# Performance work log

Measured on AMD Instinct MI355X. Metric: run time of the kernel, lower is better.

The kernel has to match this reference:

```python
import jax, jax.numpy as jnp
import numpy as np

DIM = 768
NUM_BLOCKS = 4
BLOCK = DIM // NUM_BLOCKS
SCALE = 0.02


def setup_inputs() -> dict:
    key = jax.random.key(0)
    ks = jax.random.split(key, 7)
    x = jax.random.normal(ks[0], (8, 64, 64, DIM), dtype=jnp.float32)
    w1 = SCALE * jax.random.normal(ks[1], (2, NUM_BLOCKS, BLOCK, BLOCK), dtype=jnp.float32)
    b1 = SCALE * jax.random.normal(ks[2], (2, NUM_BLOCKS, BLOCK), dtype=jnp.float32)
    w2 = SCALE * jax.random.normal(ks[3], (2, NUM_BLOCKS, BLOCK, BLOCK), dtype=jnp.float32)
    b2 = SCALE * jax.random.normal(ks[4], (2, NUM_BLOCKS, BLOCK), dtype=jnp.float32)
    # nn.Linear(dim, dim) weight/bias (kaiming-uniform-ish init; exact init irrelevant for correctness)
    lim = 1.0 / np.sqrt(DIM)
    bias_w = jax.random.uniform(ks[5], (DIM, DIM), minval=-lim, maxval=lim, dtype=jnp.float32)
    bias_b = jax.random.uniform(ks[6], (DIM,), minval=-lim, maxval=lim, dtype=jnp.float32)
    return {"x": x, "w1": w1, "b1": b1, "w2": w2, "b2": b2, "bias_w": bias_w, "bias_b": bias_b}


def _block_mul(t, w):
    # t: (..., nb, bs), w: (nb, bs, bs) -> (..., nb, bs)
    return jnp.einsum('...bd,bdk->...bk', t, w)


def reference(x, w1, b1, w2, b2, bias_w, bias_b):
    B, H, W, C = x.shape
    nb = w1.shape[1]
    bs = C // nb
    bias = x @ bias_w.T + bias_b  # nn.Linear on original x
    xb = x.reshape(B, H, W, nb, bs)
    xf = jnp.fft.rfftn(xb, axes=(1, 2), norm='ortho')  # (B, H, W//2+1, nb, bs) complex
    xr, xi = xf.real, xf.imag
    # layer 1: complex block matmul + bias + relu (relu applied per real/imag part as in source)
    r1 = jax.nn.relu(_block_mul(xr, w1[0]) - _block_mul(xi, w1[1]) + b1[0])
    i1 = jax.nn.relu(_block_mul(xr, w1[1]) + _block_mul(xi, w1[0]) + b1[1])
    # layer 2: NOTE the original torch code reassigns x_real first and then uses the NEW
    # x_real when computing x_imag — we faithfully reproduce that.
    r2 = _block_mul(r1, w2[0]) - _block_mul(i1, w2[1]) + b2[0]
    i2 = _block_mul(r2, w2[1]) + _block_mul(i1, w2[0]) + b2[1]
    xc = jax.lax.complex(r2, i2)
    out = jnp.fft.irfftn(xc, s=(H, W), axes=(1, 2), norm='ortho')
    out = out.reshape(B, H, W, C)
    return out + bias
```

## Files before the change

### kernel.cpp

```cpp
#include <hip/hip_runtime.h>

#define DIM 768
#define NBLK 4
#define BS 192
#define BATCH 8
#define HH 64
#define WW 64
#define KH 33
#define NPTS (BATCH*HH*KH)
#define TWOPI_OVER_64 0.0981747704246810387f
#define LROW 200
#define WSZ (NBLK*BS*BS)

typedef __attribute__((ext_vector_type(8))) short short8;
typedef __attribute__((ext_vector_type(4))) short short4v;
typedef __attribute__((ext_vector_type(4))) float floatx4;
typedef __attribute__((ext_vector_type(4))) unsigned int uint4v;

static __device__ __forceinline__ short f2bs(float f) {
  union { float f; unsigned int i; } v; v.f = f;
  unsigned int x = v.i;
  return (short)((x + 0x7fffu + ((x >> 16) & 1u)) >> 16);
}
static __device__ __forceinline__ float bs2f(short s) {
  union { unsigned int i; float f; } v; v.i = ((unsigned int)(unsigned short)s) << 16; return v.f;
}
static __device__ __forceinline__ short f2bs_fast(float f) {
  union { float f; unsigned int i; } v; v.f = f;
  return (short)((v.i + 0x8000u) >> 16);
}

__global__ __launch_bounds__(256) void k_bias_gemm2(
    const float* __restrict__ X, const float* __restrict__ Wt,
    const float* __restrict__ bb, float* __restrict__ out)
{
  __shared__ short As[128 * 32];
  __shared__ short Bs[128 * 32];
  const int t = threadIdx.x;
  const int wave = t >> 6, lane = t & 63;
  const int qm = lane & 15, quad = lane >> 4;
  const int wr = (wave >> 1) * 64;
  const int wc = (wave & 1) * 64;
  const int m0 = blockIdx.x * 128, n0 = blockIdx.y * 128;

  floatx4 acc[4][4];
  const floatx4 zero = {0.f, 0.f, 0.f, 0.f};
  #pragma unroll
  for (int ms = 0; ms < 4; ++ms)
    #pragma unroll
    for (int ns = 0; ns < 4; ++ns) acc[ms][ns] = zero;

  const float4* X4 = (const float4*)X;
  const float4* W4 = (const float4*)Wt;

  #pragma unroll 1
  for (int k0 = 0; k0 < DIM; k0 += 32) {
    __syncthreads();
    #pragma unroll
    for (int j = 0; j < 2; ++j) {
      const int c = t + j * 256;
      const int r = c >> 2, ko = (c & 3) * 8;
      const size_t ga = (size_t)(m0 + r) * (DIM/4) + (k0 + ko) / 4;
      const size_t gb = (size_t)(n0 + r) * (DIM/4) + (k0 + ko) / 4;
      const float4 a0 = X4[ga], a1 = X4[ga + 1];
      const float4 b0 = W4[gb], b1 = W4[gb + 1];
      short8 pa = { f2bs_fast(a0.x), f2bs_fast(a0.y), f2bs_fast(a0.z), f2bs_fast(a0.w),
                    f2bs_fast(a1.x), f2bs_fast(a1.y), f2bs_fast(a1.z), f2bs_fast(a1.w) };
      short8 pb = { f2bs_fast(b0.x), f2bs_fast(b0.y), f2bs_fast(b0.z), f2bs_fast(b0.w),
                    f2bs_fast(b1.x), f2bs_fast(b1.y), f2bs_fast(b1.z), f2bs_fast(b1.w) };
      *(short8*)&As[r * 32 + ko] = pa;
      *(short8*)&Bs[r * 32 + ko] = pb;
    }
    __syncthreads();

    short8 af[4], bf[4];
    #pragma unroll
    for (int ms = 0; ms < 4; ++ms)
      af[ms] = *(const short8*)&As[(wr + ms*16 + qm) * 32 + quad * 8];
    #pragma unroll
    for (int ns = 0; ns < 4; ++ns)
      bf[ns] = *(const short8*)&Bs[(wc + ns*16 + qm) * 32 + quad * 8];
    #pragma unroll
    for (int ms = 0; ms < 4; ++ms)
      #pragma unroll
      for (int ns = 0; ns < 4; ++ns)
        acc[ms][ns] = __builtin_amdgcn_mfma_f32_16x16x32_bf16(af[ms], bf[ns], acc[ms][ns], 0, 0, 0);
  }

  #pragma unroll
  for (int ns = 0; ns < 4; ++ns) {
    const int col = n0 + wc + ns*16 + qm;
    const float bias = bb[col];
    #pragma unroll
    for (int ms = 0; ms < 4; ++ms)
      #pragma unroll
      for (int r = 0; r < 4; ++r) {
        const int row = m0 + wr + ms*16 + quad*4 + r;
        out[(size_t)row * DIM + col] = acc[ms][ns][r] + bias;
      }
  }
}

__global__ __launch_bounds__(256) void k_rfft_w_mfma(
    const float* __restrict__ X,
    float* __restrict__ Sr, float* __restrict__ Si)
{
  __shared__ short Lx[96 * 72];
  const int t = threadIdx.x;
  const int wave = t >> 6, lane = t & 63;
  const int qm = lane & 15, quad = lane >> 4;
  const int bh = blockIdx.x;
  const int c0 = blockIdx.y * 96;
  const size_t xbase = (size_t)bh * (WW*DIM);
  const size_t obase = (size_t)bh * (KH*DIM);

  #pragma unroll
  for (int it = 0; it < 3; ++it) {
    const int i = t + it * 256;
    const int hd = i & 31;
    const int c4 = i >> 5;
    const size_t g0 = xbase + (size_t)(2*hd) * DIM + c0 + c4 * 4;
    const float4 ra = *(const float4*)&X[g0];
    const float4 rb = *(const float4*)&X[g0 + DIM];
    const float raf[4] = {ra.x, ra.y, ra.z, ra.w};
    const float rbf[4] = {rb.x, rb.y, rb.z, rb.w};
    #pragma unroll
    for (int e = 0; e < 4; ++e) {
      const int d = (c4*4 + e) * 36 + hd;
      ((unsigned*)Lx)[d] = (unsigned)(unsigned short)f2bs(raf[e]) |
                           ((unsigned)(unsigned short)f2bs(rbf[e]) << 16);
    }
  }

  short8 Trh[2], Trl[2], Tih[2], Til[2];
  const int krow = wave * 16 + qm;
  #pragma unroll
  for (int kk = 0; kk < 2; ++kk) {
    #pragma unroll
    for (int j = 0; j < 8; ++j) {
      const int w = quad * 8 + j + kk * 32;
      const int ph = (krow * w) & 63;
      float s, c;
      sincosf((float)ph * TWOPI_OVER_64, &s, &c);
      const float tr = c, ti = -s;
      const short trh = f2bs(tr);
      const short tih = f2bs(ti);
      Trh[kk][j] = trh;  Trl[kk][j] = f2bs(tr - bs2f(trh));
      Tih[kk][j] = tih;  Til[kk][j] = f2bs(ti - bs2f(tih));
    }
  }
  __syncthreads();

  if (wave < 3) {
    const floatx4 zero = {0.f, 0.f, 0.f, 0.f};
    #pragma unroll 1
    for (int ct = 0; ct < 6; ++ct) {
      floatx4 Cr = zero, Ci = zero;
      #pragma unroll
      for (int kk = 0; kk < 2; ++kk) {
        const int a = (ct*16 + qm) * 72 + kk*32 + quad*8;
        const short8 xv = *(const short8*)&Lx[a];
        Cr = __builtin_amdgcn_mfma_f32_16x16x32_bf16(Trh[kk], xv, Cr, 0,0,0);
        Cr = __builtin_amdgcn_mfma_f32_16x16x32_bf16(Trl[kk], xv, Cr, 0,0,0);
        Ci = __builtin_amdgcn_mfma_f32_16x16x32_bf16(Tih[kk], xv, Ci, 0,0,0);
        Ci = __builtin_amdgcn_mfma_f32_16x16x32_bf16(Til[kk], xv, Ci, 0,0,0);
      }
      #pragma unroll
      for (int r = 0; r < 4; ++r) {
        const int ko = wave*16 + quad*4 + r;
        if (ko < KH) {
          const size_t o = obase + (size_t)ko * DIM + c0 + ct*16 + qm;
          Sr[o] = Cr[r];
          Si[o] = Ci[r];
        }
      }
    }
  }
}

__global__ __launch_bounds__(256) void k_prep_w(
    const float* __restrict__ w1, const float* __restrict__ w2,
    short* __restrict__ Wout)
{
  const int arr = blockIdx.y;
  const int i = blockIdx.x * 256 + threadIdx.x;
  const int nb = i / (BS*BS);
  const int rem = i % (BS*BS);
  const int n = rem / BS;
  const int d = rem % BS;
  const float* src = (arr < 2) ? w1 : w2;
  const int j = arr & 1;
  const float s = (arr == 3) ? -1.f : 1.f;
  const float v = s * src[((size_t)(j*NBLK + nb) * BS + d) * BS + n];
  Wout[(size_t)arr * WSZ + i] = f2bs(v);
}

__global__ __launch_bounds__(256) void k_prep_w2(
    const float* __restrict__ w2, const float* __restrict__ b2,
    short* __restrict__ Wout, float* __restrict__ b2x)
{
  const int i = blockIdx.x * 256 + threadIdx.x;
  const int n = i % BS;
  const int d = (i / BS) % BS;
  const int nb = i / (BS*BS);
  const float* R = w2 + (size_t)nb * BS * BS;
  const float* I = w2 + ((size_t)NBLK + nb) * BS * BS;
  const float* br = b2 + nb * BS;
  float ri = 0.f, ii = 0.f, bx = 0.f;
  #pragma unroll 4
  for (int m = 0; m < BS; ++m) {
    const float win = I[m*BS + n];
    ri += R[d*BS + m] * win;
    ii += I[d*BS + m] * win;
    bx += br[m] * win;
  }
  const size_t o = ((size_t)nb * BS + n) * BS + d;
  Wout[(size_t)4 * WSZ + o] = f2bs(ri);
  Wout[(size_t)5 * WSZ + o] = f2bs(R[d*BS + n] - ii);
  if (d == 0) b2x[nb * BS + n] = b2[(NBLK + nb) * BS + n] + bx;
}

__global__ __launch_bounds__(256, 2) void k_fmix(
    float* __restrict__ Sr, float* __restrict__ Si,
    const short* __restrict__ WT,
    const float* __restrict__ b1, const float* __restrict__ b2,
    const float* __restrict__ b2x)
{
  __shared__ short U[2 * 192 * 72];
  short* Ldr = U;
  short* Ldi = U + 192 * 72;
  short* Amr = U;
  short* Ami = U + 64 * LROW;

  const int t = threadIdx.x;
  const int wave = t >> 6, lane = t & 63;
  const int qm = lane & 15, quad = lane >> 4;
  const int bk = blockIdx.x;
  const int b = bk / KH, k = bk % KH;
  const int nb = blockIdx.y;
  const int c0 = nb * BS;
  const size_t hstride = (size_t)KH * DIM;
  const size_t base = ((size_t)b * HH * KH + k) * DIM;

  short8 Ch[2], Cl[2], Sh[2], Sl[2], SNh[2], SNl[2];
  const int hp = wave * 16 + qm;
  #pragma unroll
  for (int kk = 0; kk < 2; ++kk)
    #pragma unroll
    for (int j = 0; j < 8; ++j) {
      const int h = quad*8 + j + kk*32;
      const int ph = (hp * h) & 63;
      float s, c;
      sincosf((float)ph * TWOPI_OVER_64, &s, &c);
      const short ch = f2bs(c), sh = f2bs(s);
      Ch[kk][j] = ch;  Cl[kk][j] = f2bs(c - bs2f(ch));
      Sh[kk][j] = sh;  Sl[kk][j] = f2bs(s - bs2f(sh));
      SNh[kk][j] = (short)(sh ^ (short)0x8000);
      SNl[kk][j] = (short)(Sl[kk][j] ^ (short)0x8000);
    }

  #pragma unroll
  for (int it = 0; it < 6; ++it) {
    const int i = t + it * 256;
    const int hd = i & 31;
    const int c4 = i >> 5;
    const size_t g0 = base + (size_t)(2*hd) * hstride + c0 + c4 * 4;
    const float4 ra = *(const float4*)&Sr[g0];
    const float4 rb = *(const float4*)&Sr[g0 + hstride];
    const float4 ia = *(const float4*)&Si[g0];
    const float4 ib = *(const float4*)&Si[g0 + hstride];
    const float raf[4] = {ra.x, ra.y, ra.z, ra.w};
    const float rbf[4] = {rb.x, rb.y, rb.z, rb.w};
    const float iaf[4] = {ia.x, ia.y, ia.z, ia.w};
    const float ibf[4] = {ib.x, ib.y, ib.z, ib.w};
    #pragma unroll
    for (int e = 0; e < 4; ++e) {
      const int d = (c4*4 + e) * 36 + hd;
      ((unsigned*)Ldr)[d] = (unsigned)(unsigned short)f2bs(raf[e]) |
                            ((unsigned)(unsigned short)f2bs(rbf[e]) << 16);
      ((unsigned*)Ldi)[d] = (unsigned)(unsigned short)f2bs(iaf[e]) |
                            ((unsigned)(unsigned short)f2bs(ibf[e]) << 16);
    }
  }
  __syncthreads();

  const floatx4 zero = {0.f, 0.f, 0.f, 0.f};
  floatx4 Fr[12], Fi[12];
  #pragma unroll
  for (int ct = 0; ct < 12; ++ct) { Fr[ct] = zero; Fi[ct] = zero; }
  #pragma unroll
  for (int ct = 0; ct < 12; ++ct)
    #pragma unroll
    for (int kk = 0; kk < 2; ++kk) {
      const int a = (ct*16 + qm) * 72 + kk*32 + quad*8;
      const short8 sr = *(const short8*)&Ldr[a];
      const short8 si = *(const short8*)&Ldi[a];
      Fr[ct] = __builtin_amdgcn_mfma_f32_16x16x32_bf16(Ch[kk],  sr, Fr[ct], 0,0,0);
      Fr[ct] = __builtin_amdgcn_mfma_f32_16x16x32_bf16(Cl[kk],  sr, Fr[ct], 0,0,0);
      Fr[ct] = __builtin_amdgcn_mfma_f32_16x16x32_bf16(Sh[kk],  si, Fr[ct], 0,0,0);
      Fr[ct] = __builtin_amdgcn_mfma_f32_16x16x32_bf16(Sl[kk],  si, Fr[ct], 0,0,0);
      Fi[ct] = __builtin_amdgcn_mfma_f32_16x16x32_bf16(SNh[kk], sr, Fi[ct], 0,0,0);
      Fi[ct] = __builtin_amdgcn_mfma_f32_16x16x32_bf16(SNl[kk], sr, Fi[ct], 0,0,0);
      Fi[ct] = __builtin_amdgcn_mfma_f32_16x16x32_bf16(Ch[kk],  si, Fi[ct], 0,0,0);
      Fi[ct] = __builtin_amdgcn_mfma_f32_16x16x32_bf16(Cl[kk],  si, Fi[ct], 0,0,0);
    }
  __syncthreads();

  #pragma unroll
  for (int ct = 0; ct < 12; ++ct)
    #pragma unroll
    for (int r = 0; r < 4; ++r) {
      const int row = wave*16 + quad*4 + r;
      const int c = ct*16 + qm;
      Amr[row * LROW + c] = f2bs(Fr[ct][r] * 0.015625f);
      Ami[row * LROW + c] = f2bs(Fi[ct][r] * 0.015625f);
    }
  __syncthreads();

  const short* W1R  = WT;
  const short* W1I  = WT + 1 * (size_t)WSZ;
  const short* W2R  = WT + 2 * (size_t)WSZ;
  const short* W2IN = WT + 3 * (size_t)WSZ;
  const short* W2RI = WT + 4 * (size_t)WSZ;
  const short* W2X  = WT + 5 * (size_t)WSZ;

  int nl[3];
  size_t wb[3];
  #pragma unroll
  for (int nt = 0; nt < 3; ++nt) {
    nl[nt] = wave * 48 + nt * 16 + qm;
    wb[nt] = (size_t)(c0 + nl[nt]) * BS + quad * 8;
  }

  floatx4 aR[4][3], aI[4][3];
  #pragma unroll
  for (int ms = 0; ms < 4; ++ms)
    #pragma unroll
    for (int nt = 0; nt < 3; ++nt) { aR[ms][nt] = zero; aI[ms][nt] = zero; }

  #pragma unroll 1
  for (int k0 = 0; k0 < BS; k0 += 32) {
    short8 xr[4], xi[4];
    #pragma unroll
    for (int ms = 0; ms < 4; ++ms) {
      const int a = (ms*16 + qm) * LROW + k0 + quad * 8;
      xr[ms] = *(const short8*)&Amr[a];
      xi[ms] = *(const short8*)&Ami[a];
    }
    #pragma unroll
    for (int nt = 0; nt < 3; ++nt) {
      const short8 br = *(const short8*)&W1R[wb[nt] + k0];
      const short8 bi = *(const short8*)&W1I[wb[nt] + k0];
      short8 bin;
      *(uint4v*)&bin = *(const uint4v*)&bi ^ 0x80008000u;
      #pragma unroll
      for (int ms = 0; ms < 4; ++ms) {
        aR[ms][nt] = __builtin_amdgcn_mfma_f32_16x16x32_bf16(xr[ms], br,  aR[ms][nt], 0,0,0);
        aR[ms][nt] = __builtin_amdgcn_mfma_f32_16x16x32_bf16(xi[ms], bin, aR[ms][nt], 0,0,0);
        aI[ms][nt] = __builtin_amdgcn_mfma_f32_16x16x32_bf16(xr[ms], bi,  aI[ms][nt], 0,0,0);
        aI[ms][nt] = __builtin_amdgcn_mfma_f32_16x16x32_bf16(xi[ms], br,  aI[ms][nt], 0,0,0);
      }
    }
  }
  __syncthreads();
  #pragma unroll
  for (int nt = 0; nt < 3; ++nt) {
    const float b1r = b1[nb * BS + nl[nt]];
    const float b1i = b1[(NBLK + nb) * BS + nl[nt]];
    #pragma unroll
    for (int ms = 0; ms < 4; ++ms)
      #pragma unroll
      for (int r = 0; r < 4; ++r) {
        const int row = ms*16 + quad*4 + r;
        Amr[row * LROW + nl[nt]] = f2bs(fmaxf(aR[ms][nt][r] + b1r, 0.f));
        Ami[row * LROW + nl[nt]] = f2bs(fmaxf(aI[ms][nt][r] + b1i, 0.f));
      }
  }
  __syncthreads();

  floatx4 c2r[4][3], c2i[4][3];
  #pragma unroll
  for (int ms = 0; ms < 4; ++ms)
    #pragma unroll
    for (int nt = 0; nt < 3; ++nt) { c2r[ms][nt] = zero; c2i[ms][nt] = zero; }

  #pragma unroll 1
  for (int k0 = 0; k0 < BS; k0 += 32) {
    short8 r1[4], i1[4];
    #pragma unroll
    for (int ms = 0; ms < 4; ++ms) {
      const int a = (ms*16 + qm) * LROW + k0 + quad * 8;
      r1[ms] = *(const short8*)&Amr[a];
      i1[ms] = *(const short8*)&Ami[a];
    }
    #pragma unroll
    for (int nt = 0; nt < 3; ++nt) {
      const short8 w_r  = *(const short8*)&W2R [wb[nt] + k0];
      const short8 w_in = *(const short8*)&W2IN[wb[nt] + k0];
      const short8 w_ri = *(const short8*)&W2RI[wb[nt] + k0];
      const short8 w_x  = *(const short8*)&W2X [wb[nt] + k0];
      #pragma unroll
      for (int ms = 0; ms < 4; ++ms) {
        c2r[ms][nt] = __builtin_amdgcn_mfma_f32_16x16x32_bf16(r1[ms], w_r,  c2r[ms][nt], 0,0,0);
        c2r[ms][nt] = __builtin_amdgcn_mfma_f32_16x16x32_bf16(i1[ms], w_in, c2r[ms][nt], 0,0,0);
        c2i[ms][nt] = __builtin_amdgcn_mfma_f32_16x16x32_bf16(r1[ms], w_ri, c2i[ms][nt], 0,0,0);
        c2i[ms][nt] = __builtin_amdgcn_mfma_f32_16x16x32_bf16(i1[ms], w_x,  c2i[ms][nt], 0,0,0);
      }
    }
  }
  __syncthreads();

  #pragma unroll
  for (int nt = 0; nt < 3; ++nt) {
    const float b2r = b2 [nb * BS + nl[nt]];
    const float bxi = b2x[nb * BS + nl[nt]];
    #pragma unroll
    for (int ms = 0; ms < 4; ++ms)
      #pragma unroll
      for (int r = 0; r < 4; ++r) {
        const int row = ms*16 + quad*4 + r;
        const int c = nl[nt];
        Ldr[c * 72 + row] = f2bs(c2r[ms][nt][r] + b2r);
        Ldi[c * 72 + row] = f2bs(c2i[ms][nt][r] + bxi);
      }
  }
  __syncthreads();

  #pragma unroll 1
  for (int ct = 0; ct < 12; ++ct) {
    floatx4 Cr = zero, Ci = zero;
    #pragma unroll
    for (int kk = 0; kk < 2; ++kk) {
      const int a = (ct*16 + qm) * 72 + kk*32 + quad*8;
      const short8 gr = *(const short8*)&Ldr[a];
      const short8 gi = *(const short8*)&Ldi[a];
      Cr = __builtin_amdgcn_mfma_f32_16x16x32_bf16(Ch[kk],  gr, Cr, 0,0,0);
      Cr = __builtin_amdgcn_mfma_f32_16x16x32_bf16(Cl[kk],  gr, Cr, 0,0,0);
      Cr = __builtin_amdgcn_mfma_f32_16x16x32_bf16(SNh[kk], gi, Cr, 0,0,0);
      Cr = __builtin_amdgcn_mfma_f32_16x16x32_bf16(SNl[kk], gi, Cr, 0,0,0);
      Ci = __builtin_amdgcn_mfma_f32_16x16x32_bf16(Sh[kk],  gr, Ci, 0,0,0);
      Ci = __builtin_amdgcn_mfma_f32_16x16x32_bf16(Sl[kk],  gr, Ci, 0,0,0);
      Ci = __builtin_amdgcn_mfma_f32_16x16x32_bf16(Ch[kk],  gi, Ci, 0,0,0);
      Ci = __builtin_amdgcn_mfma_f32_16x16x32_bf16(Cl[kk],  gi, Ci, 0,0,0);
    }
    #pragma unroll
    for (int r = 0; r < 4; ++r) {
      const int hpo = wave*16 + quad*4 + r;
      const size_t o = base + (size_t)hpo * hstride + c0 + ct*16 + qm;
      Sr[o] = Cr[r];
      Si[o] = Ci[r];
    }
  }
}

__global__ __launch_bounds__(256) void k_irfft_w_mfma(
    const float* __restrict__ Sr, const float* __restrict__ Si,
    float* __restrict__ out)
{
  __shared__ short Lr[96 * 72];
  __shared__ short Li[96 * 72];
  const int t = threadIdx.x;
  const int wave = t >> 6, lane = t & 63;
  const int qm = lane & 15, quad = lane >> 4;
  const int bh = blockIdx.x;
  const int c0 = blockIdx.y * 96;
  const size_t gbase = (size_t)bh * (KH*DIM);
  const size_t obase = (size_t)bh * (WW*DIM);

  #pragma unroll
  for (int it = 0; it < 3; ++it) {
    const int i = t + it * 256;
    const int hd = i & 31;
    const int c4 = i >> 5;
    const int ka = 2*hd, kb = 2*hd + 1;
    float4 ra = {0.f,0.f,0.f,0.f}, rb = ra, ia = ra, ib = ra;
    if (ka < KH) {
      const size_t g0 = gbase + (size_t)ka * DIM + c0 + c4 * 4;
      ra = *(const float4*)&Sr[g0];
      ia = *(const float4*)&Si[g0];
    }
    if (kb < KH) {
      const size_t g1 = gbase + (size_t)kb * DIM + c0 + c4 * 4;
      rb = *(const float4*)&Sr[g1];
      ib = *(const float4*)&Si[g1];
    }
    const float raf[4] = {ra.x, ra.y, ra.z, ra.w};
    const float rbf[4] = {rb.x, rb.y, rb.z, rb.w};
    const float iaf[4] = {ia.x, ia.y, ia.z, ia.w};
    const float ibf[4] = {ib.x, ib.y, ib.z, ib.w};
    #pragma unroll
    for (int e = 0; e < 4; ++e) {
      const int d = (c4*4 + e) * 36 + hd;
      ((unsigned*)Lr)[d] = (unsigned)(unsigned short)f2bs(raf[e]) |
                           ((unsigned)(unsigned short)f2bs(rbf[e]) << 16);
      ((unsigned*)Li)[d] = (unsigned)(unsigned short)f2bs(iaf[e]) |
                           ((unsigned)(unsigned short)f2bs(ibf[e]) << 16);
    }
  }

  short8 Arh[2], Arl[2], Aih[2], Ail[2];
  const int wrow = wave * 16 + qm;
  #pragma unroll
  for (int kk = 0; kk < 2; ++kk) {
    #pragma unroll
    for (int j = 0; j < 8; ++j) {
      const int k = quad * 8 + j + kk * 32;
      float ar = 0.f, ai = 0.f;
      if (k < KH) {
        const int ph = (wrow * k) & 63;
        float s, c;
        sincosf((float)ph * TWOPI_OVER_64, &s, &c);
        const float ck = (k == 0 || k == 32) ? (1.0f/64.0f) : (2.0f/64.0f);
        ar = ck * c;
        ai = -ck * s;
      }
      const short arh = f2bs(ar);
      const short aih = f2bs(ai);
      Arh[kk][j] = arh;  Arl[kk][j] = f2bs(ar - bs2f(arh));
      Aih[kk][j] = aih;  Ail[kk][j] = f2bs(ai - bs2f(aih));
    }
  }
  __syncthreads();

  const floatx4 zero = {0.f, 0.f, 0.f, 0.f};
  #pragma unroll 1
  for (int ct = 0; ct < 6; ++ct) {
    floatx4 C = zero;
    #pragma unroll
    for (int kk = 0; kk < 2; ++kk) {
      const int a = (ct*16 + qm) * 72 + kk*32 + quad*8;
      const short8 gr = *(const short8*)&Lr[a];
      const short8 gi = *(const short8*)&Li[a];
      C = __builtin_amdgcn_mfma_f32_16x16x32_bf16(Arh[kk], gr, C, 0,0,0);
      C = __builtin_amdgcn_mfma_f32_16x16x32_bf16(Arl[kk], gr, C, 0,0,0);
      C = __builtin_amdgcn_mfma_f32_16x16x32_bf16(Aih[kk], gi, C, 0,0,0);
      C = __builtin_amdgcn_mfma_f32_16x16x32_bf16(Ail[kk], gi, C, 0,0,0);
    }
    #pragma unroll
    for (int r = 0; r < 4; ++r) {
      const int w = wave*16 + quad*4 + r;
      const size_t o = obase + (size_t)w * DIM + c0 + ct*16 + qm;
      out[o] += C[r];
    }
  }
}

extern "C" void kernel_launch(void* const* d_in, const int* in_sizes, int n_in,
                              void* d_out, int out_size, void* d_ws, size_t ws_size,
                              hipStream_t stream) {
  const float* x  = (const float*)d_in[0];
  const float* w1 = (const float*)d_in[1];
  const float* b1 = (const float*)d_in[2];
  const float* w2 = (const float*)d_in[3];
  const float* b2 = (const float*)d_in[4];
  const float* bw = (const float*)d_in[5];
  const float* bb = (const float*)d_in[6];
  float* out = (float*)d_out;

  float* Sr = (float*)d_ws;
  float* Si = Sr + (size_t)NPTS * DIM;
  short* WT = (short*)(Si + (size_t)NPTS * DIM);
  float* b2x = (float*)(WT + (size_t)6 * WSZ);

  k_prep_w<<<dim3(WSZ/256, 4), 256, 0, stream>>>(w1, w2, WT);
  k_prep_w2<<<dim3(WSZ/256), 256, 0, stream>>>(w2, b2, WT, b2x);
  k_bias_gemm2<<<dim3(32768/128, DIM/128), 256, 0, stream>>>(x, bw, bb, out);
  k_rfft_w_mfma<<<dim3(BATCH*HH, DIM/96), 256, 0, stream>>>(x, Sr, Si);
  k_fmix<<<dim3(BATCH*KH, NBLK), 256, 0, stream>>>(Sr, Si, WT, b1, b2, b2x);
  k_irfft_w_mfma<<<dim3(BATCH*HH, DIM/96), 256, 0, stream>>>(Sr, Si, out);
}
```

Measured before the change: 500.8 us.

## Pre-convert x and bias weight to bf16, store spectra as bf16, async LDS loads

Adds kernels that convert x and the linear weight to bf16 once, so the bias GEMM and the forward FFT read half the bytes. The bias GEMM now fills LDS directly with global_load_lds instead of converting in registers. The intermediate spectra Sr/Si are stored as bf16 instead of fp32, halving traffic between the FFT, mixing and inverse FFT kernels. The fmix LDS layout switches to an XOR swizzle with a smaller footprint, and occupancy is raised to 3 blocks. This adds an extra pass over x, and storing intermediates in bf16 may lose some precision.

```diff
diff --git a/kernel.cpp b/kernel.cpp
--- a/kernel.cpp
+++ b/kernel.cpp
@@ -25,13 +25,37 @@
 static __device__ __forceinline__ float bs2f(short s) {
   union { unsigned int i; float f; } v; v.i = ((unsigned int)(unsigned short)s) << 16; return v.f;
 }
-static __device__ __forceinline__ short f2bs_fast(float f) {
-  union { float f; unsigned int i; } v; v.f = f;
-  return (short)((v.i + 0x8000u) >> 16);
-}
-
-__global__ __launch_bounds__(256) void k_bias_gemm2(
-    const float* __restrict__ X, const float* __restrict__ Wt,
+
+#define GLD16(gp, lp) \
+  __builtin_amdgcn_global_load_lds( \
+      (const __attribute__((address_space(1))) unsigned int*)(gp), \
+      (__attribute__((address_space(3))) unsigned int*)(lp), 16, 0, 0)
+
+__global__ __launch_bounds__(256) void k_convx(
+    const float* __restrict__ X, short* __restrict__ Xb)
+{
+  const int i = blockIdx.x * 256 + threadIdx.x;
+  const float4* X4 = (const float4*)X;
+  #pragma unroll
+  for (int it = 0; it < 12; ++it) {
+    const int idx = i + it * (2048 * 256);
+    const float4 v = X4[idx];
+    short4v p = { f2bs(v.x), f2bs(v.y), f2bs(v.z), f2bs(v.w) };
+    *(short4v*)&Xb[(size_t)idx * 4] = p;
+  }
+}
+
+__global__ __launch_bounds__(256) void k_convw(
+    const float* __restrict__ W, short* __restrict__ Wb)
+{
+  const int idx = blockIdx.x * 256 + threadIdx.x;
+  const float4 v = ((const float4*)W)[idx];
+  short4v p = { f2bs(v.x), f2bs(v.y), f2bs(v.z), f2bs(v.w) };
+  *(short4v*)&Wb[(size_t)idx * 4] = p;
+}
+
+__global__ __launch_bounds__(256) void k_bias_gemm3(
+    const short* __restrict__ Xb, const short* __restrict__ Wb,
     const float* __restrict__ bb, float* __restrict__ out)
 {
   __shared__ short As[128 * 32];
@@ -50,27 +74,24 @@
     #pragma unroll
     for (int ns = 0; ns < 4; ++ns) acc[ms][ns] = zero;
 
-  const float4* X4 = (const float4*)X;
-  const float4* W4 = (const float4*)Wt;
+  const int r0 = t >> 2,        kq0 = (t & 3) * 8;
+  const int r1 = (t + 256) >> 2, kq1 = (t & 3) * 8;
+  const short* gA0 = &Xb[(size_t)(m0 + r0) * DIM + kq0];
+  const short* gA1 = &Xb[(size_t)(m0 + r1) * DIM + kq1];
+  const short* gB0 = &Wb[(size_t)(n0 + r0) * DIM + kq0];
+  const short* gB1 = &Wb[(size_t)(n0 + r1) * DIM + kq1];
+  short* lA0 = &As[wave * 512];
+  short* lA1 = &As[wave * 512 + 2048];
+  short* lB0 = &Bs[wave * 512];
+  short* lB1 = &Bs[wave * 512 + 2048];
 
   #pragma unroll 1
   for (int k0 = 0; k0 < DIM; k0 += 32) {
     __syncthreads();
-    #pragma unroll
-    for (int j = 0; j < 2; ++j) {
-      const int c = t + j * 256;
-      const int r = c >> 2, ko = (c & 3) * 8;
-      const size_t ga = (size_t)(m0 + r) * (DIM/4) + (k0 + ko) / 4;
-      const size_t gb = (size_t)(n0 + r) * (DIM/4) + (k0 + ko) / 4;
-      const float4 a0 = X4[ga], a1 = X4[ga + 1];
-      const float4 b0 = W4[gb], b1 = W4[gb + 1];
-      short8 pa = { f2bs_fast(a0.x), f2bs_fast(a0.y), f2bs_fast(a0.z), f2bs_fast(a0.w),
-                    f2bs_fast(a1.x), f2bs_fast(a1.y), f2bs_fast(a1.z), f2bs_fast(a1.w) };
-      short8 pb = { f2bs_fast(b0.x), f2bs_fast(b0.y), f2bs_fast(b0.z), f2bs_fast(b0.w),
-                    f2bs_fast(b1.x), f2bs_fast(b1.y), f2bs_fast(b1.z), f2bs_fast(b1.w) };
-      *(short8*)&As[r * 32 + ko] = pa;
-      *(short8*)&Bs[r * 32 + ko] = pb;
-    }
+    GLD16(gA0 + k0, lA0);
+    GLD16(gA1 + k0, lA1);
+    GLD16(gB0 + k0, lB0);
+    GLD16(gB1 + k0, lB1);
     __syncthreads();
 
     short8 af[4], bf[4];
@@ -102,8 +123,8 @@
 }
 
 __global__ __launch_bounds__(256) void k_rfft_w_mfma(
-    const float* __restrict__ X,
-    float* __restrict__ Sr, float* __restrict__ Si)
+    const short* __restrict__ Xb,
+    short* __restrict__ Sr, short* __restrict__ Si)
 {
   __shared__ short Lx[96 * 72];
   const int t = threadIdx.x;
@@ -120,15 +141,13 @@
     const int hd = i & 31;
     const int c4 = i >> 5;
     const size_t g0 = xbase + (size_t)(2*hd) * DIM + c0 + c4 * 4;
-    const float4 ra = *(const float4*)&X[g0];
-    const float4 rb = *(const float4*)&X[g0 + DIM];
-    const float raf[4] = {ra.x, ra.y, ra.z, ra.w};
-    const float rbf[4] = {rb.x, rb.y, rb.z, rb.w};
+    const short4v ra = *(const short4v*)&Xb[g0];
+    const short4v rb = *(const short4v*)&Xb[g0 + DIM];
     #pragma unroll
     for (int e = 0; e < 4; ++e) {
       const int d = (c4*4 + e) * 36 + hd;
-      ((unsigned*)Lx)[d] = (unsigned)(unsigned short)f2bs(raf[e]) |
-                           ((unsigned)(unsigned short)f2bs(rbf[e]) << 16);
+      ((unsigned*)Lx)[d] = (unsigned)(unsigned short)ra[e] |
+                           ((unsigned)(unsigned short)rb[e] << 16);
     }
   }
 
@@ -170,8 +189,8 @@
         const int ko = wave*16 + quad*4 + r;
         if (ko < KH) {
           const size_t o = obase + (size_t)ko * DIM + c0 + ct*16 + qm;
-          Sr[o] = Cr[r];
-          Si[o] = Ci[r];
+          Sr[o] = f2bs(Cr[r]);
+          Si[o] = f2bs(Ci[r]);
         }
       }
     }
@@ -220,15 +239,15 @@
   if (d == 0) b2x[nb * BS + n] = b2[(NBLK + nb) * BS + n] + bx;
 }
 
-__global__ __launch_bounds__(256, 2) void k_fmix(
-    float* __restrict__ Sr, float* __restrict__ Si,
+__global__ __launch_bounds__(256, 3) void k_fmix(
+    short* __restrict__ Sr, short* __restrict__ Si,
     const short* __restrict__ WT,
     const float* __restrict__ b1, const float* __restrict__ b2,
     const float* __restrict__ b2x)
 {
-  __shared__ short U[2 * 192 * 72];
+  __shared__ short U[2 * 64 * LROW];
   short* Ldr = U;
-  short* Ldi = U + 192 * 72;
+  short* Ldi = U + 192 * 64;
   short* Amr = U;
   short* Ami = U + 64 * LROW;
 
@@ -265,21 +284,18 @@
     const int hd = i & 31;
     const int c4 = i >> 5;
     const size_t g0 = base + (size_t)(2*hd) * hstride + c0 + c4 * 4;
-    const float4 ra = *(const float4*)&Sr[g0];
-    const float4 rb = *(const float4*)&Sr[g0 + hstride];
-    const float4 ia = *(const float4*)&Si[g0];
-    const float4 ib = *(const float4*)&Si[g0 + hstride];
-    const float raf[4] = {ra.x, ra.y, ra.z, ra.w};
-    const float rbf[4] = {rb.x, rb.y, rb.z, rb.w};
-    const float iaf[4] = {ia.x, ia.y, ia.z, ia.w};
-    const float ibf[4] = {ib.x, ib.y, ib.z, ib.w};
+    const short4v ra = *(const short4v*)&Sr[g0];
+    const short4v rb = *(const short4v*)&Sr[g0 + hstride];
+    const short4v ia = *(const short4v*)&Si[g0];
+    const short4v ib = *(const short4v*)&Si[g0 + hstride];
     #pragma unroll
     for (int e = 0; e < 4; ++e) {
-      const int d = (c4*4 + e) * 36 + hd;
-      ((unsigned*)Ldr)[d] = (unsigned)(unsigned short)f2bs(raf[e]) |
-                            ((unsigned)(unsigned short)f2bs(rbf[e]) << 16);
-      ((unsigned*)Ldi)[d] = (unsigned)(unsigned short)f2bs(iaf[e]) |
-                            ((unsigned)(unsigned short)f2bs(ibf[e]) << 16);
+      const int c = c4*4 + e;
+      const int d = c * 32 + (hd ^ ((c & 7) << 2));
+      ((unsigned*)Ldr)[d] = (unsigned)(unsigned short)ra[e] |
+                            ((unsigned)(unsigned short)rb[e] << 16);
+      ((unsigned*)Ldi)[d] = (unsigned)(unsigned short)ia[e] |
+                            ((unsigned)(unsigned short)ib[e] << 16);
     }
   }
   __syncthreads();
@@ -292,7 +308,7 @@
   for (int ct = 0; ct < 12; ++ct)
     #pragma unroll
     for (int kk = 0; kk < 2; ++kk) {
-      const int a = (ct*16 + qm) * 72 + kk*32 + quad*8;
+      const int a = (ct*16 + qm) * 64 + ((kk*32 + quad*8) ^ ((qm & 7) << 3));
       const short8 sr = *(const short8*)&Ldr[a];
       const short8 si = *(const short8*)&Ldi[a];
       Fr[ct] = __builtin_amdgcn_mfma_f32_16x16x32_bf16(Ch[kk],  sr, Fr[ct], 0,0,0);
@@ -414,14 +430,15 @@
   for (int nt = 0; nt < 3; ++nt) {
     const float b2r = b2 [nb * BS + nl[nt]];
     const float bxi = b2x[nb * BS + nl[nt]];
+    const int c = nl[nt];
     #pragma unroll
     for (int ms = 0; ms < 4; ++ms)
       #pragma unroll
       for (int r = 0; r < 4; ++r) {
         const int row = ms*16 + quad*4 + r;
-        const int c = nl[nt];
-        Ldr[c * 72 + row] = f2bs(c2r[ms][nt][r] + b2r);
-        Ldi[c * 72 + row] = f2bs(c2i[ms][nt][r] + bxi);
+        const int d = c * 64 + (row ^ ((c & 7) << 3));
+        Ldr[d] = f2bs(c2r[ms][nt][r] + b2r);
+        Ldi[d] = f2bs(c2i[ms][nt][r] + bxi);
       }
   }
   __syncthreads();
@@ -431,7 +448,7 @@
     floatx4 Cr = zero, Ci = zero;
     #pragma unroll
     for (int kk = 0; kk < 2; ++kk) {
-      const int a = (ct*16 + qm) * 72 + kk*32 + quad*8;
+      const int a = (ct*16 + qm) * 64 + ((kk*32 + quad*8) ^ ((qm & 7) << 3));
       const short8 gr = *(const short8*)&Ldr[a];
       const short8 gi = *(const short8*)&Ldi[a];
       Cr = __builtin_amdgcn_mfma_f32_16x16x32_bf16(Ch[kk],  gr, Cr, 0,0,0);
@@ -447,14 +464,14 @@
     for (int r = 0; r < 4; ++r) {
       const int hpo = wave*16 + quad*4 + r;
       const size_t o = base + (size_t)hpo * hstride + c0 + ct*16 + qm;
-      Sr[o] = Cr[r];
-      Si[o] = Ci[r];
+      Sr[o] = f2bs(Cr[r]);
+      Si[o] = f2bs(Ci[r]);
     }
   }
 }
 
 __global__ __launch_bounds__(256) void k_irfft_w_mfma(
-    const float* __restrict__ Sr, const float* __restrict__ Si,
+    const short* __restrict__ Sr, const short* __restrict__ Si,
     float* __restrict__ out)
 {
   __shared__ short Lr[96 * 72];
@@ -473,28 +490,24 @@
     const int hd = i & 31;
     const int c4 = i >> 5;
     const int ka = 2*hd, kb = 2*hd + 1;
-    float4 ra = {0.f,0.f,0.f,0.f}, rb = ra, ia = ra, ib = ra;
+    short4v ra = {0,0,0,0}, rb = ra, ia = ra, ib = ra;
     if (ka < KH) {
       const size_t g0 = gbase + (size_t)ka * DIM + c0 + c4 * 4;
-      ra = *(const float4*)&Sr[g0];
-      ia = *(const float4*)&Si[g0];
+      ra = *(const short4v*)&Sr[g0];
+      ia = *(const short4v*)&Si[g0];
     }
     if (kb < KH) {
       const size_t g1 = gbase + (size_t)kb * DIM + c0 + c4 * 4;
-      rb = *(const float4*)&Sr[g1];
-      ib = *(const float4*)&Si[g1];
-    }
-    const float raf[4] = {ra.x, ra.y, ra.z, ra.w};
-    const float rbf[4] = {rb.x, rb.y, rb.z, rb.w};
-    const float iaf[4] = {ia.x, ia.y, ia.z, ia.w};
-    const float ibf[4] = {ib.x, ib.y, ib.z, ib.w};
+      rb = *(const short4v*)&Sr[g1];
+      ib = *(const short4v*)&Si[g1];
+    }
     #pragma unroll
     for (int e = 0; e < 4; ++e) {
       const int d = (c4*4 + e) * 36 + hd;
-      ((unsigned*)Lr)[d] = (unsigned)(unsigned short)f2bs(raf[e]) |
-                           ((unsigned)(unsigned short)f2bs(rbf[e]) << 16);
-      ((unsigned*)Li)[d] = (unsigned)(unsigned short)f2bs(iaf[e]) |
-                           ((unsigned)(unsigned short)f2bs(ibf[e]) << 16);
+      ((unsigned*)Lr)[d] = (unsigned)(unsigned short)ra[e] |
+                           ((unsigned)(unsigned short)rb[e] << 16);
+      ((unsigned*)Li)[d] = (unsigned)(unsigned short)ia[e] |
+                           ((unsigned)(unsigned short)ib[e] << 16);
     }
   }
 
@@ -557,15 +570,19 @@
   const float* bb = (const float*)d_in[6];
   float* out = (float*)d_out;
 
-  float* Sr = (float*)d_ws;
-  float* Si = Sr + (size_t)NPTS * DIM;
-  short* WT = (short*)(Si + (size_t)NPTS * DIM);
-  float* b2x = (float*)(WT + (size_t)6 * WSZ);
-
+  short* Sr = (short*)d_ws;
+  short* Si = Sr + (size_t)NPTS * DIM;
+  short* WT = Si + (size_t)NPTS * DIM;
+  short* Xb = WT + (size_t)6 * WSZ;
+  short* Wb = Xb + (size_t)BATCH * HH * WW * DIM;
+  float* b2x = (float*)(Wb + (size_t)DIM * DIM);
+
+  k_convx<<<2048, 256, 0, stream>>>(x, Xb);
+  k_convw<<<(DIM*DIM/4)/256, 256, 0, stream>>>(bw, Wb);
   k_prep_w<<<dim3(WSZ/256, 4), 256, 0, stream>>>(w1, w2, WT);
   k_prep_w2<<<dim3(WSZ/256), 256, 0, stream>>>(w2, b2, WT, b2x);
-  k_bias_gemm2<<<dim3(32768/128, DIM/128), 256, 0, stream>>>(x, bw, bb, out);
-  k_rfft_w_mfma<<<dim3(BATCH*HH, DIM/96), 256, 0, stream>>>(x, Sr, Si);
+  k_bias_gemm3<<<dim3(32768/128, DIM/128), 256, 0, stream>>>(Xb, Wb, bb, out);
+  k_rfft_w_mfma<<<dim3(BATCH*HH, DIM/96), 256, 0, stream>>>(Xb, Sr, Si);
   k_fmix<<<dim3(BATCH*KH, NBLK), 256, 0, stream>>>(Sr, Si, WT, b1, b2, b2x);
   k_irfft_w_mfma<<<dim3(BATCH*HH, DIM/96), 256, 0, stream>>>(Sr, Si, out);
 }
```

After: 476.9 us. 1.05x faster.

## Pre-convert x and bias weight to bf16 once, use direct global-to-LDS loads

Applied to the files above, without the earlier changes.

Adds conversion kernels that turn x and the Linear weight into bf16 copies in workspace. The bias GEMM then loads these with global_load_lds straight into shared memory, and the rFFT kernel reads the bf16 copy instead of fp32 x. This avoids converting to bf16 inside every GEMM tile and halves the bytes read by the two consumers. The cost is an extra pass over x (read fp32, write bf16) and more workspace. The GEMM also switches from fast truncating rounding to round-to-nearest-even.

```diff
diff --git a/kernel.cpp b/kernel.cpp
--- a/kernel.cpp
+++ b/kernel.cpp
@@ -25,13 +25,37 @@
 static __device__ __forceinline__ float bs2f(short s) {
   union { unsigned int i; float f; } v; v.i = ((unsigned int)(unsigned short)s) << 16; return v.f;
 }
-static __device__ __forceinline__ short f2bs_fast(float f) {
-  union { float f; unsigned int i; } v; v.f = f;
-  return (short)((v.i + 0x8000u) >> 16);
-}
-
-__global__ __launch_bounds__(256) void k_bias_gemm2(
-    const float* __restrict__ X, const float* __restrict__ Wt,
+
+#define GLD16(gp, lp) \
+  __builtin_amdgcn_global_load_lds( \
+      (const __attribute__((address_space(1))) unsigned int*)(gp), \
+      (__attribute__((address_space(3))) unsigned int*)(lp), 16, 0, 0)
+
+__global__ __launch_bounds__(256) void k_convx(
+    const float* __restrict__ X, short* __restrict__ Xb)
+{
+  const int i = blockIdx.x * 256 + threadIdx.x;
+  const float4* X4 = (const float4*)X;
+  #pragma unroll
+  for (int it = 0; it < 12; ++it) {
+    const int idx = i + it * (2048 * 256);
+    const float4 v = X4[idx];
+    short4v p = { f2bs(v.x), f2bs(v.y), f2bs(v.z), f2bs(v.w) };
+    *(short4v*)&Xb[(size_t)idx * 4] = p;
+  }
+}
+
+__global__ __launch_bounds__(256) void k_convw(
+    const float* __restrict__ W, short* __restrict__ Wb)
+{
+  const int idx = blockIdx.x * 256 + threadIdx.x;
+  const float4 v = ((const float4*)W)[idx];
+  short4v p = { f2bs(v.x), f2bs(v.y), f2bs(v.z), f2bs(v.w) };
+  *(short4v*)&Wb[(size_t)idx * 4] = p;
+}
+
+__global__ __launch_bounds__(256) void k_bias_gemm3(
+    const short* __restrict__ Xb, const short* __restrict__ Wb,
     const float* __restrict__ bb, float* __restrict__ out)
 {
   __shared__ short As[128 * 32];
@@ -50,27 +74,24 @@
     #pragma unroll
     for (int ns = 0; ns < 4; ++ns) acc[ms][ns] = zero;
 
-  const float4* X4 = (const float4*)X;
-  const float4* W4 = (const float4*)Wt;
+  const int r0 = t >> 2,        kq0 = (t & 3) * 8;
+  const int r1 = (t + 256) >> 2;
+  const short* gA0 = &Xb[(size_t)(m0 + r0) * DIM + kq0];
+  const short* gA1 = &Xb[(size_t)(m0 + r1) * DIM + kq0];
+  const short* gB0 = &Wb[(size_t)(n0 + r0) * DIM + kq0];
+  const short* gB1 = &Wb[(size_t)(n0 + r1) * DIM + kq0];
+  short* lA0 = &As[wave * 512];
+  short* lA1 = &As[wave * 512 + 2048];
+  short* lB0 = &Bs[wave * 512];
+  short* lB1 = &Bs[wave * 512 + 2048];
 
   #pragma unroll 1
   for (int k0 = 0; k0 < DIM; k0 += 32) {
     __syncthreads();
-    #pragma unroll
-    for (int j = 0; j < 2; ++j) {
-      const int c = t + j * 256;
-      const int r = c >> 2, ko = (c & 3) * 8;
-      const size_t ga = (size_t)(m0 + r) * (DIM/4) + (k0 + ko) / 4;
-      const size_t gb = (size_t)(n0 + r) * (DIM/4) + (k0 + ko) / 4;
-      const float4 a0 = X4[ga], a1 = X4[ga + 1];
-      const float4 b0 = W4[gb], b1 = W4[gb + 1];
-      short8 pa = { f2bs_fast(a0.x), f2bs_fast(a0.y), f2bs_fast(a0.z), f2bs_fast(a0.w),
-                    f2bs_fast(a1.x), f2bs_fast(a1.y), f2bs_fast(a1.z), f2bs_fast(a1.w) };
-      short8 pb = { f2bs_fast(b0.x), f2bs_fast(b0.y), f2bs_fast(b0.z), f2bs_fast(b0.w),
-                    f2bs_fast(b1.x), f2bs_fast(b1.y), f2bs_fast(b1.z), f2bs_fast(b1.w) };
-      *(short8*)&As[r * 32 + ko] = pa;
-      *(short8*)&Bs[r * 32 + ko] = pb;
-    }
+    GLD16(gA0 + k0, lA0);
+    GLD16(gA1 + k0, lA1);
+    GLD16(gB0 + k0, lB0);
+    GLD16(gB1 + k0, lB1);
     __syncthreads();
 
     short8 af[4], bf[4];
@@ -102,7 +123,7 @@
 }
 
 __global__ __launch_bounds__(256) void k_rfft_w_mfma(
-    const float* __restrict__ X,
+    const short* __restrict__ Xb,
     float* __restrict__ Sr, float* __restrict__ Si)
 {
   __shared__ short Lx[96 * 72];
@@ -120,15 +141,13 @@
     const int hd = i & 31;
     const int c4 = i >> 5;
     const size_t g0 = xbase + (size_t)(2*hd) * DIM + c0 + c4 * 4;
-    const float4 ra = *(const float4*)&X[g0];
-    const float4 rb = *(const float4*)&X[g0 + DIM];
-    const float raf[4] = {ra.x, ra.y, ra.z, ra.w};
-    const float rbf[4] = {rb.x, rb.y, rb.z, rb.w};
+    const short4v ra = *(const short4v*)&Xb[g0];
+    const short4v rb = *(const short4v*)&Xb[g0 + DIM];
     #pragma unroll
     for (int e = 0; e < 4; ++e) {
       const int d = (c4*4 + e) * 36 + hd;
-      ((unsigned*)Lx)[d] = (unsigned)(unsigned short)f2bs(raf[e]) |
-                           ((unsigned)(unsigned short)f2bs(rbf[e]) << 16);
+      ((unsigned*)Lx)[d] = (unsigned)(unsigned short)ra[e] |
+                           ((unsigned)(unsigned short)rb[e] << 16);
     }
   }
 
@@ -560,12 +579,16 @@
   float* Sr = (float*)d_ws;
   float* Si = Sr + (size_t)NPTS * DIM;
   short* WT = (short*)(Si + (size_t)NPTS * DIM);
-  float* b2x = (float*)(WT + (size_t)6 * WSZ);
-
+  short* Xb = WT + (size_t)6 * WSZ;
+  short* Wb = Xb + (size_t)BATCH * HH * WW * DIM;
+  float* b2x = (float*)(Wb + (size_t)DIM * DIM);
+
+  k_convx<<<2048, 256, 0, stream>>>(x, Xb);
+  k_convw<<<(DIM*DIM/4)/256, 256, 0, stream>>>(bw, Wb);
   k_prep_w<<<dim3(WSZ/256, 4), 256, 0, stream>>>(w1, w2, WT);
   k_prep_w2<<<dim3(WSZ/256), 256, 0, stream>>>(w2, b2, WT, b2x);
-  k_bias_gemm2<<<dim3(32768/128, DIM/128), 256, 0, stream>>>(x, bw, bb, out);
-  k_rfft_w_mfma<<<dim3(BATCH*HH, DIM/96), 256, 0, stream>>>(x, Sr, Si);
+  k_bias_gemm3<<<dim3(32768/128, DIM/128), 256, 0, stream>>>(Xb, Wb, bb, out);
+  k_rfft_w_mfma<<<dim3(BATCH*HH, DIM/96), 256, 0, stream>>>(Xb, Sr, Si);
   k_fmix<<<dim3(BATCH*KH, NBLK), 256, 0, stream>>>(Sr, Si, WT, b1, b2, b2x);
   k_irfft_w_mfma<<<dim3(BATCH*HH, DIM/96), 256, 0, stream>>>(Sr, Si, out);
 }
```

Result: faster. 483.7 us (-3.4%).
